# Performance work log

Hardware: AMD Instinct MI355X
Metric: run time of the kernel (lower is better)

## Reference

```python
import jax, jax.numpy as jnp
import numpy as np

N_NODES = 20000
N_EDGES = 320000
IN_CH = 256
HID = 128
HEADS = 4
OUT_CH = 200
NUM_GRAPHS = 64
NEG_SLOPE = 0.2


def setup_inputs() -> dict:
    key = jax.random.key(0)
    ks = jax.random.split(key, 16)
    x = jax.random.normal(ks[0], (N_NODES, IN_CH), dtype=jnp.float32)
    edge_index = jax.random.randint(ks[1], (2, N_EDGES), 0, N_NODES, dtype=jnp.int64)
    batch = jnp.sort(jax.random.randint(ks[2], (N_NODES,), 0, NUM_GRAPHS, dtype=jnp.int64))

    def lin(k, fan_in, fan_out):
        return jax.random.normal(k, (fan_in, fan_out), dtype=jnp.float32) / np.sqrt(fan_in)

    def att(k, h, c):
        return jax.random.normal(k, (h, c), dtype=jnp.float32) / np.sqrt(c)

    return {
        "x": x, "edge_index": edge_index, "batch": batch,
        "W1": lin(ks[3], IN_CH, HEADS * HID),
        "a_src1": att(ks[4], HEADS, HID), "a_dst1": att(ks[5], HEADS, HID),
        "b1": jnp.zeros((HEADS * HID,), jnp.float32),
        "W2": lin(ks[6], HEADS * HID, HEADS * HID),
        "a_src2": att(ks[7], HEADS, HID), "a_dst2": att(ks[8], HEADS, HID),
        "b2": jnp.zeros((HEADS * HID,), jnp.float32),
        "W3": lin(ks[9], HEADS * HID, HID),
        "a_src3": att(ks[10], 1, HID), "a_dst3": att(ks[11], 1, HID),
        "b3": jnp.zeros((HID,), jnp.float32),
        "fc_w": lin(ks[12], HID, OUT_CH),
        "fc_b": jnp.zeros((OUT_CH,), jnp.float32),
    }


def gat_conv(x, src, dst, W, a_src, a_dst, bias):
    """PyG GATConv (concat=True, negative_slope=0.2, self-loops appended by caller)."""
    N = x.shape[0]
    heads, out_ch = a_src.shape
    h = (x @ W).reshape(N, heads, out_ch)                 # [N,H,C]
    alpha_s = jnp.einsum('nhc,hc->nh', h, a_src)          # [N,H]
    alpha_d = jnp.einsum('nhc,hc->nh', h, a_dst)
    e = jax.nn.leaky_relu(alpha_s[src] + alpha_d[dst], NEG_SLOPE)  # [E,H]
    # segment softmax over edges sharing the same target node
    m = jax.ops.segment_max(e, dst, num_segments=N)
    e = jnp.exp(e - m[dst])
    denom = jax.ops.segment_sum(e, dst, num_segments=N)
    alpha = e / (denom[dst] + 1e-16)                      # [E,H]
    msg = h[src] * alpha[:, :, None]                      # [E,H,C]
    out = jax.ops.segment_sum(msg, dst, num_segments=N)   # [N,H,C]
    return out.reshape(N, heads * out_ch) + bias


def reference(x, edge_index, batch, W1, a_src1, a_dst1, b1,
              W2, a_src2, a_dst2, b2, W3, a_src3, a_dst3, b3, fc_w, fc_b):
    N = x.shape[0]
    loop = jnp.arange(N, dtype=edge_index.dtype)
    src = jnp.concatenate([edge_index[0], loop])
    dst = jnp.concatenate([edge_index[1], loop])

    h = jax.nn.elu(gat_conv(x, src, dst, W1, a_src1, a_dst1, b1))
    h = jax.nn.elu(gat_conv(h, src, dst, W2, a_src2, a_dst2, b2))
    h = jax.nn.elu(gat_conv(h, src, dst, W3, a_src3, a_dst3, b3))

    # global_mean_pool over graph ids
    sums = jax.ops.segment_sum(h, batch, num_segments=NUM_GRAPHS)
    cnts = jax.ops.segment_sum(jnp.ones((N,), h.dtype), batch, num_segments=NUM_GRAPHS)
    pooled = sums / jnp.maximum(cnts, 1.0)[:, None]       # [G,HID]
    # F.dropout with training=False is identity
    logits = pooled @ fc_w + fc_b                          # [G,OUT_CH]
    return logits
```

## Files before the change

### kernel.cpp

```cpp
#include <hip/hip_runtime.h>
#include <hip/hip_bf16.h>
#include <stdint.h>

#define N_NODES   20000
#define N_EDGES   320000
#define E_TOT     (N_EDGES + N_NODES)
#define IN_CH     256
#define HID       128
#define HEADS     4
#define OUT_CH    200
#define NUM_GRAPHS 64
#define M_PAD     20096

typedef __bf16 bf16_t;
typedef __bf16 bf16x8 __attribute__((ext_vector_type(8)));
typedef __bf16 bf16x2 __attribute__((ext_vector_type(2)));
typedef float  f32x4  __attribute__((ext_vector_type(4)));

__device__ __forceinline__ bool detect_bf16(const unsigned short* __restrict__ xu16) {
  int lane = threadIdx.x & 63;
  unsigned short v = xu16[2 * lane];
  int e = (v >> 7) & 0xff;
  unsigned long long b = __ballot(e >= 90 && e <= 160);
  return __popcll(b) >= 40;
}
__device__ __forceinline__ bool detect_i64(const unsigned* __restrict__ eidx) {
  int lane = threadIdx.x & 63;
  unsigned long long b = __ballot(eidx[2 * lane + 1] == 0u);
  return __popcll(b) >= 32;
}

struct SmallCvt {
  const void* src[11];
  bf16_t* dst[11];
  int n[11];
};

__global__ void cvt_wts(const void* __restrict__ W1, const void* __restrict__ W2,
                        const void* __restrict__ W3, bf16_t* __restrict__ W1T,
                        bf16_t* __restrict__ W2T, bf16_t* __restrict__ W3T,
                        SmallCvt tab, const unsigned short* __restrict__ xu16,
                        int* __restrict__ deg, float* __restrict__ psums) {
  bool isbf = detect_bf16(xu16);
  int i = blockIdx.x * 256 + threadIdx.x;
  if (i < N_NODES) deg[i] = 0;
  if (i < NUM_GRAPHS * HID) psums[i] = 0.f;
  if (i < 131072) {
    int k = i >> 9, nn = i & 511;
    bf16_t v = isbf ? ((const bf16_t*)W1)[i] : (bf16_t)((const float*)W1)[i];
    W1T[(size_t)nn * 256 + k] = v;
  } else if (i < 131072 + 262144) {
    int i2 = i - 131072;
    int k = i2 >> 9, nn = i2 & 511;
    bf16_t v = isbf ? ((const bf16_t*)W2)[i2] : (bf16_t)((const float*)W2)[i2];
    W2T[(size_t)nn * 512 + k] = v;
  } else if (i < 131072 + 262144 + 65536) {
    int i3 = i - 131072 - 262144;
    int k = i3 >> 7, nn = i3 & 127;
    bf16_t v = isbf ? ((const bf16_t*)W3)[i3] : (bf16_t)((const float*)W3)[i3];
    W3T[(size_t)nn * 512 + k] = v;
  } else {
    int j = i - 458752;
    for (int s = 0; s < 11; ++s) {
      if (j < tab.n[s]) {
        tab.dst[s][j] = isbf ? ((const bf16_t*)tab.src[s])[j]
                             : (bf16_t)((const float*)tab.src[s])[j];
        break;
      }
      j -= tab.n[s];
    }
  }
}

__global__ void cvt_ints_hist(const int* __restrict__ eidx, const int* __restrict__ batch,
                              int* __restrict__ esrc, int* __restrict__ edst,
                              int* __restrict__ b32, int* __restrict__ deg,
                              const unsigned* __restrict__ eidx_u) {
  bool i64 = detect_i64(eidx_u);
  int i = blockIdx.x * 256 + threadIdx.x;
  if (i < N_EDGES) {
    int s = i64 ? eidx[2 * i] : eidx[i];
    int d = i64 ? eidx[2 * (N_EDGES + i)] : eidx[N_EDGES + i];
    esrc[i] = s;
    edst[i] = d;
    atomicAdd(&deg[d], 1);
  }
  if (i < N_NODES) {
    b32[i] = i64 ? batch[2 * i] : batch[i];
    atomicAdd(&deg[i], 1);
  }
}

__launch_bounds__(1024)
__global__ void scan_deg_block(const int* __restrict__ deg, int* __restrict__ off,
                               int* __restrict__ cursor) {
  const int PT = 20;
  int t = threadIdx.x;
  int lane = t & 63, wid = t >> 6;
  int base = t * PT;
  int v[PT];
  int s = 0;
#pragma unroll
  for (int j = 0; j < PT; ++j) {
    int i = base + j;
    v[j] = (i < N_NODES) ? deg[i] : 0;
    s += v[j];
  }
  int x = s;
  for (int d = 1; d < 64; d <<= 1) {
    int y = __shfl_up(x, d);
    if (lane >= d) x += y;
  }
  __shared__ int wsum[16];
  if (lane == 63) wsum[wid] = x;
  __syncthreads();
  if (t < 16) {
    int y = wsum[t];
    for (int d = 1; d < 16; d <<= 1) {
      int z = __shfl_up(y, d);
      if (t >= d) y += z;
    }
    wsum[t] = y;
  }
  __syncthreads();
  int run = (wid > 0 ? wsum[wid - 1] : 0) + (x - s);
#pragma unroll
  for (int j = 0; j < PT; ++j) {
    int i = base + j;
    if (i < N_NODES) { off[i] = run; cursor[i] = 0; run += v[j]; }
  }
  if (t == 1023) off[N_NODES] = run;
}

__global__ void scatter_kernel(const int* __restrict__ esrc, const int* __restrict__ edst,
                               const int* __restrict__ off, int* __restrict__ cursor,
                               int* __restrict__ csr_src) {
  int e = blockIdx.x * 256 + threadIdx.x;
  if (e >= E_TOT) return;
  int s, d;
  if (e < N_EDGES) { s = esrc[e]; d = edst[e]; } else { s = d = e - N_EDGES; }
  int pos = off[d] + atomicAdd(&cursor[d], 1);
  csr_src[pos] = s;
}

template<bool MAYBE_F32>
__launch_bounds__(256)
__global__ void gemm_bf16(const void* __restrict__ Av, const bf16_t* __restrict__ BT,
                          bf16_t* __restrict__ C, int M, int N, int K) {
  bool isbf = MAYBE_F32 ? detect_bf16((const unsigned short*)Av) : true;
  const bf16_t* A  = (const bf16_t*)Av;
  const float*  Af = (const float*)Av;
  __shared__ bf16_t As[128 * 32];
  __shared__ bf16_t Bs[128 * 32];
  const int tid  = threadIdx.x;
  const int lane = tid & 63;
  const int w    = tid >> 6;
  const int wm   = w & 1, wn = w >> 1;
  const int bm   = blockIdx.x * 128;
  const int bn   = blockIdx.y * 128;
  const int quad = lane >> 4;
  const int l16  = lane & 15;

  f32x4 zero = {0.f, 0.f, 0.f, 0.f};
  f32x4 acc[4][4];
  for (int i = 0; i < 4; ++i)
    for (int j = 0; j < 4; ++j) acc[i][j] = zero;

  const int c0 = tid, c1 = tid + 256;
  const int r0 = c0 >> 2, s0 = c0 & 3;
  const int r1 = c1 >> 2, s1 = c1 & 3;
  int ga0 = bm + r0; if (ga0 > M - 1) ga0 = M - 1;
  int ga1 = bm + r1; if (ga1 > M - 1) ga1 = M - 1;

  for (int k0 = 0; k0 < K; k0 += 32) {
    if (!MAYBE_F32 || isbf) {
      __syncthreads();
      __builtin_amdgcn_global_load_lds(
          (const __attribute__((address_space(1))) void*)(A + (size_t)ga0 * K + k0 + s0 * 8),
          (__attribute__((address_space(3))) void*)(As + (size_t)(w * 64) * 8), 16, 0, 0);
      __builtin_amdgcn_global_load_lds(
          (const __attribute__((address_space(1))) void*)(BT + (size_t)(bn + r0) * K + k0 + s0 * 8),
          (__attribute__((address_space(3))) void*)(Bs + (size_t)(w * 64) * 8), 16, 0, 0);
      __builtin_amdgcn_global_load_lds(
          (const __attribute__((address_space(1))) void*)(A + (size_t)ga1 * K + k0 + s1 * 8),
          (__attribute__((address_space(3))) void*)(As + (size_t)(256 + w * 64) * 8), 16, 0, 0);
      __builtin_amdgcn_global_load_lds(
          (const __attribute__((address_space(1))) void*)(BT + (size_t)(bn + r1) * K + k0 + s1 * 8),
          (__attribute__((address_space(3))) void*)(Bs + (size_t)(256 + w * 64) * 8), 16, 0, 0);
      __syncthreads();
    } else {
      bf16x8 va0, va1;
      const float* p0 = Af + (size_t)ga0 * K + k0 + s0 * 8;
      const float* p1 = Af + (size_t)ga1 * K + k0 + s1 * 8;
      f32x4 l0 = *(const f32x4*)p0, h0 = *(const f32x4*)(p0 + 4);
      f32x4 l1 = *(const f32x4*)p1, h1 = *(const f32x4*)(p1 + 4);
      for (int j = 0; j < 4; ++j) {
        va0[j] = (bf16_t)l0[j]; va0[j + 4] = (bf16_t)h0[j];
        va1[j] = (bf16_t)l1[j]; va1[j + 4] = (bf16_t)h1[j];
      }
      bf16x8 vb0 = *(const bf16x8*)(BT + (size_t)(bn + r0) * K + k0 + s0 * 8);
      bf16x8 vb1 = *(const bf16x8*)(BT + (size_t)(bn + r1) * K + k0 + s1 * 8);
      __syncthreads();
      *(bf16x8*)(As + c0 * 8) = va0;
      *(bf16x8*)(Bs + c0 * 8) = vb0;
      *(bf16x8*)(As + c1 * 8) = va1;
      *(bf16x8*)(Bs + c1 * 8) = vb1;
      __syncthreads();
    }

    bf16x8 af[4], bfr[4];
    for (int mt = 0; mt < 4; ++mt) {
      int m_local = wm * 64 + mt * 16 + l16;
      af[mt] = *(const bf16x8*)(As + m_local * 32 + quad * 8);
    }
    for (int nt = 0; nt < 4; ++nt) {
      int n_local = wn * 64 + nt * 16 + l16;
      bfr[nt] = *(const bf16x8*)(Bs + n_local * 32 + quad * 8);
    }
    for (int mt = 0; mt < 4; ++mt)
      for (int nt = 0; nt < 4; ++nt)
        acc[mt][nt] = __builtin_amdgcn_mfma_f32_16x16x32_bf16(af[mt], bfr[nt], acc[mt][nt], 0, 0, 0);
  }

  for (int mt = 0; mt < 4; ++mt) {
    for (int r = 0; r < 4; ++r) {
      int m = bm + wm * 64 + mt * 16 + quad * 4 + r;
      if (m >= M) continue;
      for (int nt = 0; nt < 4; ++nt) {
        int n = bn + wn * 64 + nt * 16 + l16;
        C[(size_t)m * N + n] = (bf16_t)acc[mt][nt][r];
      }
    }
  }
}

template<int CPL>
__launch_bounds__(256)
__global__ void alpha_k(const bf16_t* __restrict__ h, const bf16_t* __restrict__ a_src,
                        const bf16_t* __restrict__ a_dst, float* __restrict__ as,
                        float* __restrict__ ad, int H) {
  typedef __bf16 vec_t __attribute__((ext_vector_type(CPL)));
  const int C = CPL * 64;
  int lane = threadIdx.x & 63;
  int n = blockIdx.x * 4 + (threadIdx.x >> 6);
  if (n >= N_NODES) return;
  int c0 = lane * CPL;
  vec_t hv  = *(const vec_t*)(h + (size_t)n * C + c0);
  vec_t sv  = *(const vec_t*)(a_src + c0);
  vec_t dv  = *(const vec_t*)(a_dst + c0);
  float s = 0.f, d = 0.f;
  for (int j = 0; j < CPL; ++j) {
    float hvf = (float)hv[j];
    s += hvf * (float)sv[j];
    d += hvf * (float)dv[j];
  }
  const int lph = 128 / CPL;
  for (int o = 1; o < lph; o <<= 1) {
    s += __shfl_xor(s, o);
    d += __shfl_xor(d, o);
  }
  if ((lane & (lph - 1)) == 0) {
    int hd = c0 >> 7;
    as[n * H + hd] = s;
    ad[n * H + hd] = d;
  }
}

template<int CPL>
__launch_bounds__(256)
__global__ void agg_fused(const bf16_t* __restrict__ h, const int* __restrict__ off,
                          const int* __restrict__ csr_src, const float* __restrict__ as,
                          const float* __restrict__ ad, const bf16_t* __restrict__ bias,
                          bf16_t* __restrict__ outp, int H) {
  typedef __bf16 vec_t __attribute__((ext_vector_type(CPL)));
  const int C = CPL * 64;
  int lane = threadIdx.x & 63;
  int n = blockIdx.x * 4 + (threadIdx.x >> 6);
  if (n >= N_NODES) return;
  int start = __builtin_amdgcn_readfirstlane(off[n]);
  int end   = __builtin_amdgcn_readfirstlane(off[n + 1]);
  int c0 = lane * CPL;
  int hd = c0 >> 7;
  float adv = ad[n * H + hd];
  float acc[CPL];
  for (int j = 0; j < CPL; ++j) acc[j] = 0.f;
  float den = 0.f;

  int pos = start;
  for (; pos + 3 < end; pos += 4) {
    int s0 = __builtin_amdgcn_readfirstlane(csr_src[pos]);
    int s1 = __builtin_amdgcn_readfirstlane(csr_src[pos + 1]);
    int s2 = __builtin_amdgcn_readfirstlane(csr_src[pos + 2]);
    int s3 = __builtin_amdgcn_readfirstlane(csr_src[pos + 3]);
    vec_t hv0 = *(const vec_t*)(h + (size_t)s0 * C + c0);
    vec_t hv1 = *(const vec_t*)(h + (size_t)s1 * C + c0);
    vec_t hv2 = *(const vec_t*)(h + (size_t)s2 * C + c0);
    vec_t hv3 = *(const vec_t*)(h + (size_t)s3 * C + c0);
    float e0 = as[s0 * H + hd] + adv; e0 = e0 > 0.f ? e0 : 0.2f * e0;
    float e1 = as[s1 * H + hd] + adv; e1 = e1 > 0.f ? e1 : 0.2f * e1;
    float e2 = as[s2 * H + hd] + adv; e2 = e2 > 0.f ? e2 : 0.2f * e2;
    float e3 = as[s3 * H + hd] + adv; e3 = e3 > 0.f ? e3 : 0.2f * e3;
    float w0 = __expf(e0), w1 = __expf(e1), w2 = __expf(e2), w3 = __expf(e3);
    den += (w0 + w1) + (w2 + w3);
    for (int j = 0; j < CPL; ++j)
      acc[j] += (w0 * (float)hv0[j] + w1 * (float)hv1[j])
              + (w2 * (float)hv2[j] + w3 * (float)hv3[j]);
  }
  for (; pos < end; ++pos) {
    int s0 = __builtin_amdgcn_readfirstlane(csr_src[pos]);
    vec_t hv0 = *(const vec_t*)(h + (size_t)s0 * C + c0);
    float e0 = as[s0 * H + hd] + adv; e0 = e0 > 0.f ? e0 : 0.2f * e0;
    float w0 = __expf(e0);
    den += w0;
    for (int j = 0; j < CPL; ++j) acc[j] += w0 * (float)hv0[j];
  }

  float inv = 1.f / (den + 1e-16f);
  vec_t ov;
  for (int j = 0; j < CPL; ++j) {
    float o = acc[j] * inv + (float)bias[c0 + j];
    o = o > 0.f ? o : expm1f(o);
    ov[j] = (bf16_t)o;
  }
  *(vec_t*)(outp + (size_t)n * C + c0) = ov;
}

__launch_bounds__(256)
__global__ void pool_partial(const bf16_t* __restrict__ h3, const int* __restrict__ batch,
                             float* __restrict__ psums) {
  int wave = threadIdx.x >> 6;
  int lane = threadIdx.x & 63;
  int c0 = lane * 2;
  int nbase = blockIdx.x * 128;
  int nend = nbase + 128; if (nend > N_NODES) nend = N_NODES;
  float a0 = 0.f, a1 = 0.f;
  int cur = -1;
  for (int n = nbase + wave; n < nend; n += 4) {
    int g = __builtin_amdgcn_readfirstlane(batch[n]);
    if (g != cur) {
      if (cur >= 0) {
        atomicAdd(&psums[cur * HID + c0], a0);
        atomicAdd(&psums[cur * HID + c0 + 1], a1);
      }
      cur = g; a0 = 0.f; a1 = 0.f;
    }
    bf16x2 v = *(const bf16x2*)(h3 + (size_t)n * HID + c0);
    a0 += (float)v[0];
    a1 += (float)v[1];
  }
  if (cur >= 0) {
    atomicAdd(&psums[cur * HID + c0], a0);
    atomicAdd(&psums[cur * HID + c0 + 1], a1);
  }
}

__launch_bounds__(256)
__global__ void fc_final(const float* __restrict__ psums, const int* __restrict__ batch,
                         const bf16_t* __restrict__ fcw, const bf16_t* __restrict__ fcb,
                         void* __restrict__ outp, const unsigned short* __restrict__ xu16) {
  bool isbf = detect_bf16(xu16);
  int g = blockIdx.x;
  int lo = 0, hi = N_NODES;
  while (lo < hi) { int mid = (lo + hi) >> 1; if (batch[mid] < g) lo = mid + 1; else hi = mid; }
  int start = lo;
  hi = N_NODES;
  while (lo < hi) { int mid = (lo + hi) >> 1; if (batch[mid] < g + 1) lo = mid + 1; else hi = mid; }
  int cnt = lo - start;
  __shared__ float pooled[HID];
  int t = threadIdx.x;
  if (t < HID) {
    pooled[t] = psums[g * HID + t] / (float)(cnt > 0 ? cnt : 1);
  }
  __syncthreads();
  if (t < OUT_CH) {
    float a = (float)fcb[t];
    for (int c = 0; c < HID; ++c) a += pooled[c] * (float)fcw[c * OUT_CH + t];
    if (isbf) ((bf16_t*)outp)[g * OUT_CH + t] = (bf16_t)a;
    else      ((float*)outp)[g * OUT_CH + t] = a;
  }
}

extern "C" void kernel_launch(void* const* d_in, const int* in_sizes, int n_in,
                              void* d_out, int out_size, void* d_ws, size_t ws_size,
                              hipStream_t stream) {
  const void* x    = d_in[0];
  const void* eidx = d_in[1];
  const void* batch= d_in[2];
  const void* W1   = d_in[3];
  const void* a_s1 = d_in[4];
  const void* a_d1 = d_in[5];
  const void* b1   = d_in[6];
  const void* W2   = d_in[7];
  const void* a_s2 = d_in[8];
  const void* a_d2 = d_in[9];
  const void* b2   = d_in[10];
  const void* W3   = d_in[11];
  const void* a_s3 = d_in[12];
  const void* a_d3 = d_in[13];
  const void* b3   = d_in[14];
  const void* fcw  = d_in[15];
  const void* fcb  = d_in[16];
  const unsigned short* xu16 = (const unsigned short*)x;

  char* p = (char*)d_ws;
  auto carve = [&](size_t nbytes) { char* r = p; p += (nbytes + 255) & ~(size_t)255; return r; };
  bf16_t*   W1T    = (bf16_t*)carve((size_t)512 * 256 * 2);
  bf16_t*   W2T    = (bf16_t*)carve((size_t)512 * 512 * 2);
  bf16_t*   W3T    = (bf16_t*)carve((size_t)128 * 512 * 2);
  bf16_t*   hA     = (bf16_t*)carve((size_t)M_PAD * 512 * 2);
  bf16_t*   hB     = (bf16_t*)carve((size_t)M_PAD * 512 * 2);
  bf16_t*   sm     = (bf16_t*)carve((size_t)32768 * 2);
  bf16_t *as1b = sm, *ad1b = sm + 512, *b1b = sm + 1024,
         *as2b = sm + 1536, *ad2b = sm + 2048, *b2b = sm + 2560,
         *as3b = sm + 3072, *ad3b = sm + 3200, *b3b = sm + 3328,
         *fcwb = sm + 3456, *fcbb = sm + 29056;
  float*    asb    = (float*)carve((size_t)N_NODES * 4 * 4);
  float*    adb    = (float*)carve((size_t)N_NODES * 4 * 4);
  int*      deg    = (int*)carve((size_t)N_NODES * 4);
  int*      off    = (int*)carve((size_t)(N_NODES + 1) * 4);
  int*      cursor = (int*)carve((size_t)N_NODES * 4);
  int*      csr_src= (int*)carve((size_t)E_TOT * 4);
  int*      esrc32 = (int*)carve((size_t)N_EDGES * 4);
  int*      edst32 = (int*)carve((size_t)N_EDGES * 4);
  int*      bat32  = (int*)carve((size_t)N_NODES * 4);
  float*    psums  = (float*)carve((size_t)NUM_GRAPHS * HID * 4);

  dim3 b256(256);
  const int NG4 = (N_NODES + 3) / 4;

  SmallCvt tab;
  const void* srcs[11] = {a_s1, a_d1, b1, a_s2, a_d2, b2, a_s3, a_d3, b3, fcw, fcb};
  bf16_t* dsts[11] = {as1b, ad1b, b1b, as2b, ad2b, b2b, as3b, ad3b, b3b, fcwb, fcbb};
  int ns[11] = {512, 512, 512, 512, 512, 512, 128, 128, 128, 25600, 200};
  for (int i = 0; i < 11; ++i) { tab.src[i] = srcs[i]; tab.dst[i] = dsts[i]; tab.n[i] = ns[i]; }
  cvt_wts<<<dim3((458752 + 29256 + 255) / 256), b256, 0, stream>>>(
      W1, W2, W3, W1T, W2T, W3T, tab, xu16, deg, psums);
  cvt_ints_hist<<<dim3((N_EDGES + 255) / 256), b256, 0, stream>>>(
      (const int*)eidx, (const int*)batch, esrc32, edst32, bat32, deg, (const unsigned*)eidx);

  scan_deg_block<<<dim3(1), dim3(1024), 0, stream>>>(deg, off, cursor);
  scatter_kernel<<<dim3((E_TOT + 255) / 256), b256, 0, stream>>>(esrc32, edst32, off, cursor, csr_src);

  gemm_bf16<true><<<dim3(157, 4), b256, 0, stream>>>(x, W1T, hA, N_NODES, 512, 256);
  alpha_k<8><<<dim3(NG4), b256, 0, stream>>>(hA, as1b, ad1b, asb, adb, 4);
  agg_fused<8><<<dim3(NG4), b256, 0, stream>>>(hA, off, csr_src, asb, adb, b1b, hB, 4);

  gemm_bf16<false><<<dim3(157, 4), b256, 0, stream>>>(hB, W2T, hA, N_NODES, 512, 512);
  alpha_k<8><<<dim3(NG4), b256, 0, stream>>>(hA, as2b, ad2b, asb, adb, 4);
  agg_fused<8><<<dim3(NG4), b256, 0, stream>>>(hA, off, csr_src, asb, adb, b2b, hB, 4);

  gemm_bf16<false><<<dim3(157, 1), b256, 0, stream>>>(hB, W3T, hA, N_NODES, 128, 512);
  alpha_k<2><<<dim3(NG4), b256, 0, stream>>>(hA, as3b, ad3b, asb, adb, 1);
  agg_fused<2><<<dim3(NG4), b256, 0, stream>>>(hA, off, csr_src, asb, adb, b3b, hB, 1);

  pool_partial<<<dim3((N_NODES + 127) / 128), b256, 0, stream>>>(hB, bat32, psums);
  fc_final<<<dim3(NUM_GRAPHS), b256, 0, stream>>>(psums, bat32, fcwb, fcbb, d_out, xu16);
}
```

Baseline: 366.7 us.

## Fuse attention logits into GEMM epilogue and merge prep and pooling kernels

Computes the per-node attention dot products (alpha_src/alpha_dst) in the GEMM epilogue from fp32 accumulators, so the separate alpha kernels and their re-read of h are gone. Merges the weight-conversion and edge-conversion/histogram kernels into one prep kernel, with a memset zeroing degrees. Folds mean pooling into the final FC kernel using per-graph binary-searched ranges instead of atomics. This cuts launches and memory passes, but pooling now runs on only 64 blocks, and the logits come from fp32 accumulators rather than rounded bf16 h.

```diff
diff --git a/kernel.cpp b/kernel.cpp
--- a/kernel.cpp
+++ b/kernel.cpp
@@ -36,15 +36,27 @@
   int n[11];
 };
 
-__global__ void cvt_wts(const void* __restrict__ W1, const void* __restrict__ W2,
-                        const void* __restrict__ W3, bf16_t* __restrict__ W1T,
-                        bf16_t* __restrict__ W2T, bf16_t* __restrict__ W3T,
-                        SmallCvt tab, const unsigned short* __restrict__ xu16,
-                        int* __restrict__ deg, float* __restrict__ psums) {
+__global__ void prep(const void* __restrict__ W1, const void* __restrict__ W2,
+                     const void* __restrict__ W3, bf16_t* __restrict__ W1T,
+                     bf16_t* __restrict__ W2T, bf16_t* __restrict__ W3T,
+                     SmallCvt tab, const unsigned short* __restrict__ xu16,
+                     const int* __restrict__ eidx, const int* __restrict__ batch,
+                     int* __restrict__ esrc, int* __restrict__ edst,
+                     int* __restrict__ b32, int* __restrict__ deg) {
   bool isbf = detect_bf16(xu16);
+  bool i64  = detect_i64((const unsigned*)eidx);
   int i = blockIdx.x * 256 + threadIdx.x;
-  if (i < N_NODES) deg[i] = 0;
-  if (i < NUM_GRAPHS * HID) psums[i] = 0.f;
+  if (i < N_EDGES) {
+    int s = i64 ? eidx[2 * i] : eidx[i];
+    int d = i64 ? eidx[2 * (N_EDGES + i)] : eidx[N_EDGES + i];
+    esrc[i] = s;
+    edst[i] = d;
+    atomicAdd(&deg[d], 1);
+  }
+  if (i < N_NODES) {
+    b32[i] = i64 ? batch[2 * i] : batch[i];
+    atomicAdd(&deg[i], 1);
+  }
   if (i < 131072) {
     int k = i >> 9, nn = i & 511;
     bf16_t v = isbf ? ((const bf16_t*)W1)[i] : (bf16_t)((const float*)W1)[i];
@@ -72,25 +84,6 @@
   }
 }
 
-__global__ void cvt_ints_hist(const int* __restrict__ eidx, const int* __restrict__ batch,
-                              int* __restrict__ esrc, int* __restrict__ edst,
-                              int* __restrict__ b32, int* __restrict__ deg,
-                              const unsigned* __restrict__ eidx_u) {
-  bool i64 = detect_i64(eidx_u);
-  int i = blockIdx.x * 256 + threadIdx.x;
-  if (i < N_EDGES) {
-    int s = i64 ? eidx[2 * i] : eidx[i];
-    int d = i64 ? eidx[2 * (N_EDGES + i)] : eidx[N_EDGES + i];
-    esrc[i] = s;
-    edst[i] = d;
-    atomicAdd(&deg[d], 1);
-  }
-  if (i < N_NODES) {
-    b32[i] = i64 ? batch[2 * i] : batch[i];
-    atomicAdd(&deg[i], 1);
-  }
-}
-
 __launch_bounds__(1024)
 __global__ void scan_deg_block(const int* __restrict__ deg, int* __restrict__ off,
                                int* __restrict__ cursor) {
@@ -146,12 +139,16 @@
 template<bool MAYBE_F32>
 __launch_bounds__(256)
 __global__ void gemm_bf16(const void* __restrict__ Av, const bf16_t* __restrict__ BT,
-                          bf16_t* __restrict__ C, int M, int N, int K) {
+                          bf16_t* __restrict__ C, int M, int N, int K,
+                          const bf16_t* __restrict__ a_src, const bf16_t* __restrict__ a_dst,
+                          float* __restrict__ as, float* __restrict__ ad, int H) {
   bool isbf = MAYBE_F32 ? detect_bf16((const unsigned short*)Av) : true;
   const bf16_t* A  = (const bf16_t*)Av;
   const float*  Af = (const float*)Av;
   __shared__ bf16_t As[128 * 32];
   __shared__ bf16_t Bs[128 * 32];
+  __shared__ float sred[2][128];
+  __shared__ float dred[2][128];
   const int tid  = threadIdx.x;
   const int lane = tid & 63;
   const int w    = tid >> 6;
@@ -160,6 +157,7 @@
   const int bn   = blockIdx.y * 128;
   const int quad = lane >> 4;
   const int l16  = lane & 15;
+  const int hd   = bn >> 7;
 
   f32x4 zero = {0.f, 0.f, 0.f, 0.f};
   f32x4 acc[4][4];
@@ -232,37 +230,37 @@
       }
     }
   }
-}
-
-template<int CPL>
-__launch_bounds__(256)
-__global__ void alpha_k(const bf16_t* __restrict__ h, const bf16_t* __restrict__ a_src,
-                        const bf16_t* __restrict__ a_dst, float* __restrict__ as,
-                        float* __restrict__ ad, int H) {
-  typedef __bf16 vec_t __attribute__((ext_vector_type(CPL)));
-  const int C = CPL * 64;
-  int lane = threadIdx.x & 63;
-  int n = blockIdx.x * 4 + (threadIdx.x >> 6);
-  if (n >= N_NODES) return;
-  int c0 = lane * CPL;
-  vec_t hv  = *(const vec_t*)(h + (size_t)n * C + c0);
-  vec_t sv  = *(const vec_t*)(a_src + c0);
-  vec_t dv  = *(const vec_t*)(a_dst + c0);
-  float s = 0.f, d = 0.f;
-  for (int j = 0; j < CPL; ++j) {
-    float hvf = (float)hv[j];
-    s += hvf * (float)sv[j];
-    d += hvf * (float)dv[j];
-  }
-  const int lph = 128 / CPL;
-  for (int o = 1; o < lph; o <<= 1) {
-    s += __shfl_xor(s, o);
-    d += __shfl_xor(d, o);
-  }
-  if ((lane & (lph - 1)) == 0) {
-    int hd = c0 >> 7;
-    as[n * H + hd] = s;
-    ad[n * H + hd] = d;
+
+  float av[4], dv[4];
+  for (int nt = 0; nt < 4; ++nt) {
+    int ch = wn * 64 + nt * 16 + l16;
+    av[nt] = (float)a_src[hd * 128 + ch];
+    dv[nt] = (float)a_dst[hd * 128 + ch];
+  }
+  for (int mt = 0; mt < 4; ++mt) {
+    for (int r = 0; r < 4; ++r) {
+      float s = acc[mt][0][r] * av[0] + acc[mt][1][r] * av[1]
+              + acc[mt][2][r] * av[2] + acc[mt][3][r] * av[3];
+      float d = acc[mt][0][r] * dv[0] + acc[mt][1][r] * dv[1]
+              + acc[mt][2][r] * dv[2] + acc[mt][3][r] * dv[3];
+      for (int o = 1; o < 16; o <<= 1) {
+        s += __shfl_xor(s, o);
+        d += __shfl_xor(d, o);
+      }
+      if (l16 == 0) {
+        int row_local = wm * 64 + mt * 16 + quad * 4 + r;
+        sred[wn][row_local] = s;
+        dred[wn][row_local] = d;
+      }
+    }
+  }
+  __syncthreads();
+  if (tid < 128) {
+    int m = bm + tid;
+    if (m < M) {
+      as[m * H + hd] = sred[0][tid] + sred[1][tid];
+      ad[m * H + hd] = dred[0][tid] + dred[1][tid];
+    }
   }
 }
 
@@ -326,36 +324,7 @@
 }
 
 __launch_bounds__(256)
-__global__ void pool_partial(const bf16_t* __restrict__ h3, const int* __restrict__ batch,
-                             float* __restrict__ psums) {
-  int wave = threadIdx.x >> 6;
-  int lane = threadIdx.x & 63;
-  int c0 = lane * 2;
-  int nbase = blockIdx.x * 128;
-  int nend = nbase + 128; if (nend > N_NODES) nend = N_NODES;
-  float a0 = 0.f, a1 = 0.f;
-  int cur = -1;
-  for (int n = nbase + wave; n < nend; n += 4) {
-    int g = __builtin_amdgcn_readfirstlane(batch[n]);
-    if (g != cur) {
-      if (cur >= 0) {
-        atomicAdd(&psums[cur * HID + c0], a0);
-        atomicAdd(&psums[cur * HID + c0 + 1], a1);
-      }
-      cur = g; a0 = 0.f; a1 = 0.f;
-    }
-    bf16x2 v = *(const bf16x2*)(h3 + (size_t)n * HID + c0);
-    a0 += (float)v[0];
-    a1 += (float)v[1];
-  }
-  if (cur >= 0) {
-    atomicAdd(&psums[cur * HID + c0], a0);
-    atomicAdd(&psums[cur * HID + c0 + 1], a1);
-  }
-}
-
-__launch_bounds__(256)
-__global__ void fc_final(const float* __restrict__ psums, const int* __restrict__ batch,
+__global__ void pool_fc2(const bf16_t* __restrict__ h3, const int* __restrict__ batch,
                          const bf16_t* __restrict__ fcw, const bf16_t* __restrict__ fcb,
                          void* __restrict__ outp, const unsigned short* __restrict__ xu16) {
   bool isbf = detect_bf16(xu16);
@@ -365,11 +334,25 @@
   int start = lo;
   hi = N_NODES;
   while (lo < hi) { int mid = (lo + hi) >> 1; if (batch[mid] < g + 1) lo = mid + 1; else hi = mid; }
-  int cnt = lo - start;
+  int end = lo, cnt = end - start;
+
+  int t = threadIdx.x;
+  int wave = t >> 6, lane = t & 63;
+  int c0 = lane * 2;
+  float a0 = 0.f, a1 = 0.f;
+  for (int n = start + wave; n < end; n += 4) {
+    bf16x2 v = *(const bf16x2*)(h3 + (size_t)n * HID + c0);
+    a0 += (float)v[0];
+    a1 += (float)v[1];
+  }
+  __shared__ float red[4][HID];
+  red[wave][c0] = a0;
+  red[wave][c0 + 1] = a1;
+  __syncthreads();
   __shared__ float pooled[HID];
-  int t = threadIdx.x;
   if (t < HID) {
-    pooled[t] = psums[g * HID + t] / (float)(cnt > 0 ? cnt : 1);
+    float s = red[0][t] + red[1][t] + red[2][t] + red[3][t];
+    pooled[t] = s / (float)(cnt > 0 ? cnt : 1);
   }
   __syncthreads();
   if (t < OUT_CH) {
@@ -423,7 +406,6 @@
   int*      esrc32 = (int*)carve((size_t)N_EDGES * 4);
   int*      edst32 = (int*)carve((size_t)N_EDGES * 4);
   int*      bat32  = (int*)carve((size_t)N_NODES * 4);
-  float*    psums  = (float*)carve((size_t)NUM_GRAPHS * HID * 4);
 
   dim3 b256(256);
   const int NG4 = (N_NODES + 3) / 4;
@@ -433,26 +415,26 @@
   bf16_t* dsts[11] = {as1b, ad1b, b1b, as2b, ad2b, b2b, as3b, ad3b, b3b, fcwb, fcbb};
   int ns[11] = {512, 512, 512, 512, 512, 512, 128, 128, 128, 25600, 200};
   for (int i = 0; i < 11; ++i) { tab.src[i] = srcs[i]; tab.dst[i] = dsts[i]; tab.n[i] = ns[i]; }
-  cvt_wts<<<dim3((458752 + 29256 + 255) / 256), b256, 0, stream>>>(
-      W1, W2, W3, W1T, W2T, W3T, tab, xu16, deg, psums);
-  cvt_ints_hist<<<dim3((N_EDGES + 255) / 256), b256, 0, stream>>>(
-      (const int*)eidx, (const int*)batch, esrc32, edst32, bat32, deg, (const unsigned*)eidx);
+
+  hipMemsetAsync(deg, 0, (size_t)N_NODES * 4, stream);
+  prep<<<dim3((458752 + 29256 + 255) / 256), b256, 0, stream>>>(
+      W1, W2, W3, W1T, W2T, W3T, tab, xu16,
+      (const int*)eidx, (const int*)batch, esrc32, edst32, bat32, deg);
 
   scan_deg_block<<<dim3(1), dim3(1024), 0, stream>>>(deg, off, cursor);
   scatter_kernel<<<dim3((E_TOT + 255) / 256), b256, 0, stream>>>(esrc32, edst32, off, cursor, csr_src);
 
-  gemm_bf16<true><<<dim3(157, 4), b256, 0, stream>>>(x, W1T, hA, N_NODES, 512, 256);
-  alpha_k<8><<<dim3(NG4), b256, 0, stream>>>(hA, as1b, ad1b, asb, adb, 4);
+  gemm_bf16<true><<<dim3(157, 4), b256, 0, stream>>>(x, W1T, hA, N_NODES, 512, 256,
+                                                     as1b, ad1b, asb, adb, 4);
   agg_fused<8><<<dim3(NG4), b256, 0, stream>>>(hA, off, csr_src, asb, adb, b1b, hB, 4);
 
-  gemm_bf16<false><<<dim3(157, 4), b256, 0, stream>>>(hB, W2T, hA, N_NODES, 512, 512);
-  alpha_k<8><<<dim3(NG4), b256, 0, stream>>>(hA, as2b, ad2b, asb, adb, 4);
+  gemm_bf16<false><<<dim3(157, 4), b256, 0, stream>>>(hB, W2T, hA, N_NODES, 512, 512,
+                                                      as2b, ad2b, asb, adb, 4);
   agg_fused<8><<<dim3(NG4), b256, 0, stream>>>(hA, off, csr_src, asb, adb, b2b, hB, 4);
 
-  gemm_bf16<false><<<dim3(157, 1), b256, 0, stream>>>(hB, W3T, hA, N_NODES, 128, 512);
-  alpha_k<2><<<dim3(NG4), b256, 0, stream>>>(hA, as3b, ad3b, asb, adb, 1);
+  gemm_bf16<false><<<dim3(157, 1), b256, 0, stream>>>(hB, W3T, hA, N_NODES, 128, 512,
+                                                      as3b, ad3b, asb, adb, 1);
   agg_fused<2><<<dim3(NG4), b256, 0, stream>>>(hA, off, csr_src, asb, adb, b3b, hB, 1);
 
-  pool_partial<<<dim3((N_NODES + 127) / 128), b256, 0, stream>>>(hB, bat32, psums);
-  fc_final<<<dim3(NUM_GRAPHS), b256, 0, stream>>>(psums, bat32, fcwb, fcbb, d_out, xu16);
-}
+  pool_fc2<<<dim3(NUM_GRAPHS), b256, 0, stream>>>(hB, bat32, fcwb, fcbb, d_out, xu16);
+}
```

New measurement: 370.8 us. No clear change (+1.1%).
